# Kernel tuning notes

Hardware: AMD Instinct MI355X
Metric: run time of the kernel (lower is better)

## Reference

```python
import jax, jax.numpy as jnp
import numpy as np

NEG_SLOPE = 0.2


def _gat(x, src, dst, W, a_src, a_dst, b, N):
    # PyG GATConv (eval mode, concat=True). W: [Fin, H*C], a_*: [H, C], b: [H*C]
    H, C = a_src.shape
    h = (x @ W).reshape(N, H, C)                       # [N,H,C]
    al_s = jnp.einsum('nhc,hc->nh', h, a_src)          # source attention logits
    al_d = jnp.einsum('nhc,hc->nh', h, a_dst)          # target attention logits
    e = jax.nn.leaky_relu(al_s[src] + al_d[dst], NEG_SLOPE)  # [E,H]
    m = jax.ops.segment_max(e, dst, num_segments=N)
    m = jnp.where(jnp.isneginf(m), 0.0, m)
    p = jnp.exp(e - m[dst])
    s = jax.ops.segment_sum(p, dst, num_segments=N)
    alpha = p / (s[dst] + 1e-16)                       # segment softmax over incoming edges
    out = jax.ops.segment_sum(h[src] * alpha[:, :, None], dst, num_segments=N)
    return out.reshape(N, H * C) + b


def _lin(key, fin, fout):
    k1, k2 = jax.random.split(key)
    w = jax.random.normal(k1, (fin, fout), jnp.float32) / np.sqrt(fin)
    b = jax.random.normal(k2, (fout,), jnp.float32) * 0.01
    return w, b


def _gat_params(key, fin, H, C):
    k1, k2, k3, k4 = jax.random.split(key, 4)
    W = jax.random.normal(k1, (fin, H * C), jnp.float32) / np.sqrt(fin)
    a_s = jax.random.normal(k2, (H, C), jnp.float32) / np.sqrt(C)
    a_d = jax.random.normal(k3, (H, C), jnp.float32) / np.sqrt(C)
    b = jax.random.normal(k4, (H * C,), jnp.float32) * 0.01
    return W, a_s, a_d, b


def setup_inputs() -> dict:
    key = jax.random.key(0)
    N, E, F, HID, H = 20000, 320000, 128, 128, 2
    W_ = HID * H  # 256
    ks = jax.random.split(key, 12)
    x = jax.random.normal(ks[0], (N, F), jnp.float32)
    edge_index = jax.random.randint(ks[1], (2, E), 0, N, jnp.int64)
    edge_attr = jax.random.normal(ks[2], (E, 4), jnp.float32)
    ec_w1, ec_b1 = _lin(ks[3], 2 * F, HID)
    ec_w2, ec_b2 = _lin(ks[4], HID, HID)
    g1 = _gat_params(ks[5], HID, H, HID)
    g2 = _gat_params(ks[6], W_, H, HID)
    reg_w, reg_b = _lin(ks[7], W_, W_)
    g3 = _gat_params(ks[8], W_, H, HID)
    g4 = _gat_params(ks[9], W_, H, HID)
    fin_w, fin_b = _lin(ks[10], W_, 1)
    d = {"x": x, "edge_index": edge_index, "edge_attr": edge_attr,
         "ec_w1": ec_w1, "ec_b1": ec_b1, "ec_w2": ec_w2, "ec_b2": ec_b2,
         "reg_w": reg_w, "reg_b": reg_b, "fin_w": fin_w, "fin_b": fin_b}
    for name, p in (("g1", g1), ("g2", g2), ("g3", g3), ("g4", g4)):
        d[name + "_w"], d[name + "_as"], d[name + "_ad"], d[name + "_b"] = p
    return d


def reference(x, edge_index, edge_attr,
              ec_w1, ec_b1, ec_w2, ec_b2,
              g1_w, g1_as, g1_ad, g1_b,
              g2_w, g2_as, g2_ad, g2_b,
              reg_w, reg_b,
              g3_w, g3_as, g3_ad, g3_b,
              g4_w, g4_as, g4_ad, g4_b,
              fin_w, fin_b):
    N = x.shape[0]
    src, dst = edge_index[0], edge_index[1]
    # EdgeConv: msg = MLP([x_i, x_j - x_i]), max-aggregation at target i (no self loops)
    xi = x[dst]
    msg = jnp.concatenate([xi, x[src] - xi], axis=-1)          # [E, 2F]
    h = jnp.maximum(msg @ ec_w1 + ec_b1, 0.0) @ ec_w2 + ec_b2   # [E, HID]
    agg = jax.ops.segment_max(h, dst, num_segments=N)
    x = jnp.where(jnp.isneginf(agg), 0.0, agg)
    # GATConv adds self loops by default
    loop = jnp.arange(N, dtype=src.dtype)
    s2 = jnp.concatenate([src, loop])
    d2 = jnp.concatenate([dst, loop])
    # edge_attr is ignored by GATConv (edge_dim=None)
    x = jax.nn.relu(_gat(x, s2, d2, g1_w, g1_as, g1_ad, g1_b, N))
    r = x
    x = jax.nn.relu(_gat(x, s2, d2, g2_w, g2_as, g2_ad, g2_b, N)) + r
    x = x @ reg_w + reg_b
    r = x
    x = jax.nn.relu(_gat(x, s2, d2, g3_w, g3_as, g3_ad, g3_b, N)) + r
    x = jax.nn.relu(_gat(x, s2, d2, g4_w, g4_as, g4_ad, g4_b, N))
    return x @ fin_w + fin_b
```

## Files before the change

kernel.cpp:

```cpp
#include <hip/hip_runtime.h>
#include <math.h>


#define NEG_SLOPE 0.2f

typedef short short8 __attribute__((ext_vector_type(8)));
typedef float float4v __attribute__((ext_vector_type(4)));
typedef unsigned short ushort4v __attribute__((ext_vector_type(4)));

#define AS1 __attribute__((address_space(1)))
#define AS3 __attribute__((address_space(3)))

__device__ __forceinline__ void cp16(const void* g, void* l) {
  __builtin_amdgcn_global_load_lds((const AS1 unsigned int*)g, (AS3 unsigned int*)l, 16, 0, 0);
}

__device__ __forceinline__ float leaky(float x) { return x > 0.f ? x : NEG_SLOPE * x; }

__device__ __forceinline__ void atomicMaxF(float* addr, float v) {
  if (v >= 0.f) atomicMax((int*)addr, __float_as_int(v));
  else          atomicMin((unsigned int*)addr, __float_as_uint(v));
}

__device__ __forceinline__ unsigned short bf16_rn(float f) {
  unsigned u = __float_as_uint(f);
  unsigned r = (u + 0x7FFFu + ((u >> 16) & 1u)) >> 16;
  return (unsigned short)r;
}
__device__ __forceinline__ float bf16_to_f(unsigned short h) {
  return __uint_as_float(((unsigned)h) << 16);
}
__device__ __forceinline__ float4 ld_bf4(const unsigned short* p) {
  ushort4v u = *(const ushort4v*)p;
  float4 f;
  f.x = bf16_to_f(u[0]); f.y = bf16_to_f(u[1]);
  f.z = bf16_to_f(u[2]); f.w = bf16_to_f(u[3]);
  return f;
}

__global__ __launch_bounds__(256) void k_fill_f32(float* p, float v, int n) {
  int i = blockIdx.x * 256 + threadIdx.x;
  if (i < n) p[i] = v;
}

__global__ __launch_bounds__(256) void k_split_act(const float* __restrict__ src,
                                                   unsigned short* __restrict__ h,
                                                   unsigned short* __restrict__ l,
                                                   int n, int fixinf) {
  int i4 = (blockIdx.x * 256 + threadIdx.x) * 4;
  if (i4 >= n) return;
  float4 v = *(const float4*)&src[i4];
  if (fixinf) {
    if (v.x == -INFINITY) v.x = 0.f;
    if (v.y == -INFINITY) v.y = 0.f;
    if (v.z == -INFINITY) v.z = 0.f;
    if (v.w == -INFINITY) v.w = 0.f;
  }
  unsigned short hx = bf16_rn(v.x), hy = bf16_rn(v.y), hz = bf16_rn(v.z), hw = bf16_rn(v.w);
  ushort4v h4 = {hx, hy, hz, hw};
  ushort4v l4 = {bf16_rn(v.x - bf16_to_f(hx)), bf16_rn(v.y - bf16_to_f(hy)),
                 bf16_rn(v.z - bf16_to_f(hz)), bf16_rn(v.w - bf16_to_f(hw))};
  *(ushort4v*)&h[i4] = h4;
  *(ushort4v*)&l[i4] = l4;
}

__global__ __launch_bounds__(256) void k_hist(const int* __restrict__ ei, int* __restrict__ deg,
                                              int E) {
  int e = blockIdx.x * 256 + threadIdx.x;
  if (e < E) atomicAdd(&deg[ei[E + e]], 1);
}

__global__ __launch_bounds__(1024) void k_scan(const int* __restrict__ deg, int* __restrict__ rs,
                                               int n) {
  __shared__ int wsum[16];
  __shared__ int carry;
  int tid = threadIdx.x, lane = tid & 63, wv = tid >> 6;
  if (tid == 0) carry = 0;
  __syncthreads();
  for (int base = 0; base < n; base += 1024) {
    int i = base + tid;
    int v = (i < n) ? deg[i] : 0;
    int s = v;
    #pragma unroll
    for (int o = 1; o < 64; o <<= 1) {
      int t = __shfl(s, lane - o);
      if (lane >= o) s += t;
    }
    if (lane == 63) wsum[wv] = s;
    __syncthreads();
    if (wv == 0) {
      int x = (lane < 16) ? wsum[lane] : 0;
      #pragma unroll
      for (int o = 1; o < 16; o <<= 1) {
        int t = __shfl(x, lane - o);
        if (lane >= o) x += t;
      }
      if (lane < 16) wsum[lane] = x;
    }
    __syncthreads();
    int woff = carry + (wv ? wsum[wv - 1] : 0);
    if (i < n) rs[i] = woff + s - v;
    __syncthreads();
    if (tid == 0) carry += wsum[15];
    __syncthreads();
  }
  if (tid == 0) rs[n] = carry;
}

__global__ __launch_bounds__(256) void k_scatter(const int* __restrict__ ei,
                                                 const int* __restrict__ rs,
                                                 int* __restrict__ cnt,
                                                 int* __restrict__ csr_src,
                                                 int* __restrict__ csr_dst, int E) {
  int e = blockIdx.x * 256 + threadIdx.x;
  if (e < E) {
    int d = ei[E + e];
    int p = atomicAdd(&cnt[d], 1);
    int slot = rs[d] + p;
    csr_src[slot] = ei[e];
    csr_dst[slot] = d;
  }
}

struct SplitJob {
  const float* W;
  const float* aux;
  unsigned short* Th;
  unsigned short* Tl;
  float* bias_out;
  int K, N, kshift, type;
};
struct SplitJobs { SplitJob j[7]; };

__global__ __launch_bounds__(256) void k_prep_all(SplitJobs jobs) {
  SplitJob jb = jobs.j[blockIdx.y];
  int idx = blockIdx.x * 256 + threadIdx.x;
  if (idx >= jb.K * jb.N) return;
  float v;
  if (jb.type == 0) {
    int n = idx >> jb.kshift;
    int k = idx & (jb.K - 1);
    v = jb.W[k * jb.N + n];
  } else {
    int n = idx >> 7;
    int k = idx & 127;
    if (n < 128) v = jb.W[k * 128 + n] - jb.W[(k + 128) * 128 + n];
    else         v = jb.W[(k + 128) * 128 + (n - 128)];
    if (idx < 256) jb.bias_out[idx] = (idx < 128) ? jb.aux[idx] : 0.f;
  }
  unsigned short h = bf16_rn(v);
  jb.Th[idx] = h;
  jb.Tl[idx] = bf16_rn(v - bf16_to_f(h));
}

__global__ __launch_bounds__(256) void k_gemm_mfma(const unsigned short* __restrict__ Ah,
                                                   const unsigned short* __restrict__ Al,
                                                   const unsigned short* __restrict__ BTh,
                                                   const unsigned short* __restrict__ BTl,
                                                   const float* __restrict__ bias,
                                                   float* __restrict__ C, int M, int K,
                                                   unsigned short* __restrict__ Ch,
                                                   unsigned short* __restrict__ Cl,
                                                   unsigned short* __restrict__ Cbf,
                                                   const float* __restrict__ a_s,
                                                   const float* __restrict__ a_d,
                                                   float* __restrict__ al_out) {
  __shared__ __align__(16) char sm[24576];
  __shared__ float alS[64][2];
  char* AhS = sm;
  char* AlS = sm + 4096;
  char* BhS = sm + 8192;
  char* BlS = sm + 16384;

  const int tid = threadIdx.x;
  const int bm = blockIdx.x * 64;
  const int bn = blockIdx.y * 128;
  const int w = tid >> 6, lane = tid & 63, quad = lane >> 4, lr = lane & 15;
  const int kq8 = quad * 8;

  float4v zero4 = {0.f, 0.f, 0.f, 0.f};
  float4v acc[4][2];
  #pragma unroll
  for (int mt = 0; mt < 4; ++mt)
    #pragma unroll
    for (int nt = 0; nt < 2; ++nt) acc[mt][nt] = zero4;

  int ar = bm + w * 16 + lr; if (ar >= M) ar = M - 1;
  const size_t aoff  = (size_t)ar * K + kq8;
  const size_t boff0 = (size_t)(bn + (2 * w) * 16 + lr) * K + kq8;
  const size_t boff1 = (size_t)(bn + (2 * w + 1) * 16 + lr) * K + kq8;
  char* lA   = AhS + w * 1024;
  char* lAl  = AlS + w * 1024;
  char* lB0  = BhS + (2 * w) * 1024;
  char* lB1  = BhS + (2 * w + 1) * 1024;
  char* lBl0 = BlS + (2 * w) * 1024;
  char* lBl1 = BlS + (2 * w + 1) * 1024;

  for (int k0 = 0; k0 < K; k0 += 32) {
    __syncthreads();
    cp16(Ah + aoff + k0, lA);
    cp16(Al + aoff + k0, lAl);
    cp16(BTh + boff0 + k0, lB0);
    cp16(BTh + boff1 + k0, lB1);
    cp16(BTl + boff0 + k0, lBl0);
    cp16(BTl + boff1 + k0, lBl1);
    __syncthreads();
    short8 ah[4], alo[4], bh[2], blo[2];
    #pragma unroll
    for (int mt = 0; mt < 4; ++mt) {
      ah[mt]  = *(const short8*)(AhS + mt * 1024 + lane * 16);
      alo[mt] = *(const short8*)(AlS + mt * 1024 + lane * 16);
    }
    #pragma unroll
    for (int nt = 0; nt < 2; ++nt) {
      bh[nt]  = *(const short8*)(BhS + (2 * w + nt) * 1024 + lane * 16);
      blo[nt] = *(const short8*)(BlS + (2 * w + nt) * 1024 + lane * 16);
    }
    #pragma unroll
    for (int mt = 0; mt < 4; ++mt)
      #pragma unroll
      for (int nt = 0; nt < 2; ++nt) {
        acc[mt][nt] = __builtin_amdgcn_mfma_f32_16x16x32_bf16(ah[mt], bh[nt], acc[mt][nt], 0, 0, 0);
        acc[mt][nt] = __builtin_amdgcn_mfma_f32_16x16x32_bf16(alo[mt], bh[nt], acc[mt][nt], 0, 0, 0);
        acc[mt][nt] = __builtin_amdgcn_mfma_f32_16x16x32_bf16(ah[mt], blo[nt], acc[mt][nt], 0, 0, 0);
      }
  }
  #pragma unroll
  for (int nt = 0; nt < 2; ++nt) {
    int n = bn + w * 32 + nt * 16 + lr;
    float bv = bias ? bias[n] : 0.f;
    #pragma unroll
    for (int mt = 0; mt < 4; ++mt) {
      #pragma unroll
      for (int r = 0; r < 4; ++r) {
        int m = bm + mt * 16 + quad * 4 + r;
        if (m < M) {
          float v = acc[mt][nt][r] + bv;
          size_t idx = (size_t)m * 256 + n;
          if (C) C[idx] = v;
          if (Cbf) Cbf[idx] = bf16_rn(v);
          if (Ch) {
            unsigned short h = bf16_rn(v);
            Ch[idx] = h;
            Cl[idx] = bf16_rn(v - bf16_to_f(h));
          }
        }
      }
    }
  }
  if (a_s) {
    if (tid < 128) ((float*)alS)[tid] = 0.f;
    __syncthreads();
    float asv[2], adv[2];
    #pragma unroll
    for (int nt = 0; nt < 2; ++nt) {
      int n = bn + w * 32 + nt * 16 + lr;
      asv[nt] = a_s[n];
      adv[nt] = a_d[n];
    }
    #pragma unroll
    for (int mt = 0; mt < 4; ++mt) {
      #pragma unroll
      for (int r = 0; r < 4; ++r) {
        float ps = acc[mt][0][r] * asv[0] + acc[mt][1][r] * asv[1];
        float pd = acc[mt][0][r] * adv[0] + acc[mt][1][r] * adv[1];
        #pragma unroll
        for (int o = 8; o; o >>= 1) {
          ps += __shfl_xor(ps, o);
          pd += __shfl_xor(pd, o);
        }
        if (lr == 0) {
          int row = mt * 16 + quad * 4 + r;
          atomicAdd(&alS[row][0], ps);
          atomicAdd(&alS[row][1], pd);
        }
      }
    }
    __syncthreads();
    int head = bn >> 7;
    if (tid < 64) {
      int m = bm + tid;
      if (m < M) {
        al_out[m * 4 + head]     = alS[tid][0];
        al_out[m * 4 + 2 + head] = alS[tid][1];
      }
    }
  }
}

__global__ __launch_bounds__(256, 4) void k_edgeconv2(const float* __restrict__ uv,
                                                      const int* __restrict__ csr_src,
                                                      const int* __restrict__ csr_dst,
                                                      const unsigned short* __restrict__ w2Th,
                                                      const unsigned short* __restrict__ w2Tl,
                                                      const float* __restrict__ b2,
                                                      float* __restrict__ x0, int E) {
  __shared__ __align__(16) char smem[34816];
  unsigned short (*Ph)[136] = (unsigned short(*)[136])smem;
  unsigned short (*Pl)[136] = (unsigned short(*)[136])(smem + 17408);
  float (*H2)[132] = (float(*)[132])smem;
  __shared__ int sSrc[64], sDst[64];

  const int tid = threadIdx.x;
  const int e0 = blockIdx.x * 64;
  const int w = tid >> 6, lane = tid & 63, quad = lane >> 4, lr = lane & 15;
  if (tid < 64) {
    int e = e0 + tid;
    sSrc[tid] = (e < E) ? csr_src[e] : -1;
    sDst[tid] = (e < E) ? csr_dst[e] : -1;
  }
  __syncthreads();
  #pragma unroll
  for (int c = tid; c < 1024; c += 256) {
    int r = c >> 4;
    int kq = (c & 15) * 8;
    float pv[8];
    int sn = sSrc[r], dn = sDst[r];
    if (sn >= 0) {
      float4 u0 = *(const float4*)&uv[(size_t)dn * 256 + kq];
      float4 u1 = *(const float4*)&uv[(size_t)dn * 256 + kq + 4];
      float4 v0 = *(const float4*)&uv[(size_t)sn * 256 + 128 + kq];
      float4 v1 = *(const float4*)&uv[(size_t)sn * 256 + 128 + kq + 4];
      pv[0] = fmaxf(u0.x + v0.x, 0.f); pv[1] = fmaxf(u0.y + v0.y, 0.f);
      pv[2] = fmaxf(u0.z + v0.z, 0.f); pv[3] = fmaxf(u0.w + v0.w, 0.f);
      pv[4] = fmaxf(u1.x + v1.x, 0.f); pv[5] = fmaxf(u1.y + v1.y, 0.f);
      pv[6] = fmaxf(u1.z + v1.z, 0.f); pv[7] = fmaxf(u1.w + v1.w, 0.f);
    } else {
      #pragma unroll
      for (int i = 0; i < 8; ++i) pv[i] = 0.f;
    }
    short8 h8, l8;
    #pragma unroll
    for (int i = 0; i < 8; ++i) {
      unsigned short h = bf16_rn(pv[i]);
      h8[i] = (short)h;
      l8[i] = (short)bf16_rn(pv[i] - bf16_to_f(h));
    }
    *(short8*)&Ph[r][kq] = h8;
    *(short8*)&Pl[r][kq] = l8;
  }
  __syncthreads();
  float4v zero4 = {0.f, 0.f, 0.f, 0.f};
  float4v acc[4][2];
  #pragma unroll
  for (int mt = 0; mt < 4; ++mt)
    #pragma unroll
    for (int nt = 0; nt < 2; ++nt) acc[mt][nt] = zero4;

  #pragma unroll
  for (int k0 = 0; k0 < 128; k0 += 32) {
    short8 ah[4], alo[4], bh[2], blo[2];
    #pragma unroll
    for (int nt = 0; nt < 2; ++nt) {
      int n = w * 32 + nt * 16 + lr;
      bh[nt]  = *(const short8*)&w2Th[(size_t)n * 128 + k0 + quad * 8];
      blo[nt] = *(const short8*)&w2Tl[(size_t)n * 128 + k0 + quad * 8];
    }
    #pragma unroll
    for (int mt = 0; mt < 4; ++mt) {
      ah[mt]  = *(short8*)&Ph[mt * 16 + lr][k0 + quad * 8];
      alo[mt] = *(short8*)&Pl[mt * 16 + lr][k0 + quad * 8];
    }
    #pragma unroll
    for (int mt = 0; mt < 4; ++mt)
      #pragma unroll
      for (int nt = 0; nt < 2; ++nt) {
        acc[mt][nt] = __builtin_amdgcn_mfma_f32_16x16x32_bf16(ah[mt], bh[nt], acc[mt][nt], 0, 0, 0);
        acc[mt][nt] = __builtin_amdgcn_mfma_f32_16x16x32_bf16(alo[mt], bh[nt], acc[mt][nt], 0, 0, 0);
        acc[mt][nt] = __builtin_amdgcn_mfma_f32_16x16x32_bf16(ah[mt], blo[nt], acc[mt][nt], 0, 0, 0);
      }
  }
  __syncthreads();
  #pragma unroll
  for (int nt = 0; nt < 2; ++nt) {
    int n = w * 32 + nt * 16 + lr;
    float bv = b2[n];
    #pragma unroll
    for (int mt = 0; mt < 4; ++mt) {
      #pragma unroll
      for (int r = 0; r < 4; ++r) {
        int row = mt * 16 + quad * 4 + r;
        H2[row][n] = acc[mt][nt][r] + bv;
      }
    }
  }
  __syncthreads();
  {
    int half = tid >> 7;
    int col = tid & 127;
    int r0 = half * 32;
    int prev = sDst[r0];
    float rmax = H2[r0][col];
    for (int r = r0 + 1; r < r0 + 32; ++r) {
      int d = sDst[r];
      float v = H2[r][col];
      if (d == prev) {
        rmax = fmaxf(rmax, v);
      } else {
        if (prev >= 0) atomicMaxF(&x0[(size_t)prev * 128 + col], rmax);
        prev = d;
        rmax = v;
      }
    }
    if (prev >= 0) atomicMaxF(&x0[(size_t)prev * 128 + col], rmax);
  }
}

__global__ __launch_bounds__(256) void k_gat_agg(const unsigned short* __restrict__ Hfb,
                                                 const float* __restrict__ al,
                                                 const int* __restrict__ rs,
                                                 const int* __restrict__ csr_src,
                                                 const float* __restrict__ bias,
                                                 const float* __restrict__ res,
                                                 float* __restrict__ out,
                                                 unsigned short* __restrict__ outh,
                                                 unsigned short* __restrict__ outl,
                                                 const float* __restrict__ finw,
                                                 const float* __restrict__ finb, int N) {
  int wave = threadIdx.x >> 6, lane = threadIdx.x & 63;
  int i = blockIdx.x * 4 + wave;
  if (i >= N) return;
  int beg = rs[i], end = rs[i + 1];
  int deg = end - beg;
  float4 me = *(const float4*)&al[i * 4];
  float ad0 = me.z, ad1 = me.w;
  float sl0 = leaky(me.x + ad0);
  float sl1 = leaky(me.y + ad1);
  const int c = lane << 2;
  const int hsel = lane >> 5;
  float a0, a1, a2, a3;

  if (deg <= 64) {
    int s = 0;
    float l0 = -INFINITY, l1 = -INFINITY;
    bool act = lane < deg;
    if (act) {
      s = csr_src[beg + lane];
      float4 a4 = *(const float4*)&al[s * 4];
      l0 = leaky(a4.x + ad0);
      l1 = leaky(a4.y + ad1);
    }
    float m0 = fmaxf(sl0, l0), m1 = fmaxf(sl1, l1);
    #pragma unroll
    for (int o = 32; o; o >>= 1) {
      m0 = fmaxf(m0, __shfl_xor(m0, o));
      m1 = fmaxf(m1, __shfl_xor(m1, o));
    }
    float w0 = act ? __expf(l0 - m0) : 0.f;
    float w1 = act ? __expf(l1 - m1) : 0.f;
    float s0 = w0, s1 = w1;
    #pragma unroll
    for (int o = 32; o; o >>= 1) {
      s0 += __shfl_xor(s0, o);
      s1 += __shfl_xor(s1, o);
    }
    s0 += __expf(sl0 - m0);
    s1 += __expf(sl1 - m1);
    float inv0 = 1.f / (s0 + 1e-16f), inv1 = 1.f / (s1 + 1e-16f);
    float wp0 = w0 * inv0, wp1 = w1 * inv1;
    float wself = hsel ? __expf(sl1 - m1) * inv1 : __expf(sl0 - m0) * inv0;
    float4 hv = ld_bf4(&Hfb[(size_t)i * 256 + c]);
    a0 = wself * hv.x; a1 = wself * hv.y; a2 = wself * hv.z; a3 = wself * hv.w;
    float b0 = 0.f, b1 = 0.f, b2 = 0.f, b3 = 0.f;
    float c0 = 0.f, c1 = 0.f, c2 = 0.f, c3 = 0.f;
    float d0 = 0.f, d1 = 0.f, d2 = 0.f, d3 = 0.f;
    int j = 0;
    for (; j + 8 <= deg; j += 8) {
      int   sjj[8];
      float wjj[8];
      #pragma unroll
      for (int q = 0; q < 8; ++q) {
        sjj[q] = __shfl(s, j + q);
        float wA = __shfl(wp0, j + q);
        float wB = __shfl(wp1, j + q);
        wjj[q] = hsel ? wB : wA;
      }
      float4 h0 = ld_bf4(&Hfb[(size_t)sjj[0] * 256 + c]);
      float4 h1 = ld_bf4(&Hfb[(size_t)sjj[1] * 256 + c]);
      float4 h2 = ld_bf4(&Hfb[(size_t)sjj[2] * 256 + c]);
      float4 h3 = ld_bf4(&Hfb[(size_t)sjj[3] * 256 + c]);
      float4 h4 = ld_bf4(&Hfb[(size_t)sjj[4] * 256 + c]);
      float4 h5 = ld_bf4(&Hfb[(size_t)sjj[5] * 256 + c]);
      float4 h6 = ld_bf4(&Hfb[(size_t)sjj[6] * 256 + c]);
      float4 h7 = ld_bf4(&Hfb[(size_t)sjj[7] * 256 + c]);
      a0 += wjj[0] * h0.x; a1 += wjj[0] * h0.y; a2 += wjj[0] * h0.z; a3 += wjj[0] * h0.w;
      b0 += wjj[1] * h1.x; b1 += wjj[1] * h1.y; b2 += wjj[1] * h1.z; b3 += wjj[1] * h1.w;
      c0 += wjj[2] * h2.x; c1 += wjj[2] * h2.y; c2 += wjj[2] * h2.z; c3 += wjj[2] * h2.w;
      d0 += wjj[3] * h3.x; d1 += wjj[3] * h3.y; d2 += wjj[3] * h3.z; d3 += wjj[3] * h3.w;
      a0 += wjj[4] * h4.x; a1 += wjj[4] * h4.y; a2 += wjj[4] * h4.z; a3 += wjj[4] * h4.w;
      b0 += wjj[5] * h5.x; b1 += wjj[5] * h5.y; b2 += wjj[5] * h5.z; b3 += wjj[5] * h5.w;
      c0 += wjj[6] * h6.x; c1 += wjj[6] * h6.y; c2 += wjj[6] * h6.z; c3 += wjj[6] * h6.w;
      d0 += wjj[7] * h7.x; d1 += wjj[7] * h7.y; d2 += wjj[7] * h7.z; d3 += wjj[7] * h7.w;
    }
    for (; j < deg; ++j) {
      int sj = __shfl(s, j);
      float wA = __shfl(wp0, j);
      float wB = __shfl(wp1, j);
      float wj = hsel ? wB : wA;
      float4 h4 = ld_bf4(&Hfb[(size_t)sj * 256 + c]);
      a0 += wj * h4.x; a1 += wj * h4.y; a2 += wj * h4.z; a3 += wj * h4.w;
    }
    a0 += b0 + c0 + d0; a1 += b1 + c1 + d1;
    a2 += b2 + c2 + d2; a3 += b3 + c3 + d3;
  } else {
    float m0 = sl0, m1 = sl1;
    for (int e = beg + lane; e < end; e += 64) {
      int s = csr_src[e];
      m0 = fmaxf(m0, leaky(al[s * 4 + 0] + ad0));
      m1 = fmaxf(m1, leaky(al[s * 4 + 1] + ad1));
    }
    #pragma unroll
    for (int o = 32; o; o >>= 1) {
      m0 = fmaxf(m0, __shfl_xor(m0, o));
      m1 = fmaxf(m1, __shfl_xor(m1, o));
    }
    float s0 = 0.f, s1 = 0.f;
    for (int e = beg + lane; e < end; e += 64) {
      int s = csr_src[e];
      s0 += __expf(leaky(al[s * 4 + 0] + ad0) - m0);
      s1 += __expf(leaky(al[s * 4 + 1] + ad1) - m1);
    }
    #pragma unroll
    for (int o = 32; o; o >>= 1) {
      s0 += __shfl_xor(s0, o);
      s1 += __shfl_xor(s1, o);
    }
    s0 += __expf(sl0 - m0);
    s1 += __expf(sl1 - m1);
    float inv0 = 1.f / (s0 + 1e-16f), inv1 = 1.f / (s1 + 1e-16f);
    float mh = hsel ? m1 : m0;
    float invh = hsel ? inv1 : inv0;
    float adh = hsel ? ad1 : ad0;
    float wself = __expf((hsel ? sl1 : sl0) - mh) * invh;
    float4 hv = ld_bf4(&Hfb[(size_t)i * 256 + c]);
    a0 = wself * hv.x; a1 = wself * hv.y; a2 = wself * hv.z; a3 = wself * hv.w;
    for (int e = beg; e < end; ++e) {
      int s = csr_src[e];
      float wgt = __expf(leaky(al[s * 4 + hsel] + adh) - mh) * invh;
      float4 h4 = ld_bf4(&Hfb[(size_t)s * 256 + c]);
      a0 += wgt * h4.x; a1 += wgt * h4.y; a2 += wgt * h4.z; a3 += wgt * h4.w;
    }
  }
  float4 bv = *(const float4*)&bias[c];
  float4 o4;
  o4.x = fmaxf(a0 + bv.x, 0.f);
  o4.y = fmaxf(a1 + bv.y, 0.f);
  o4.z = fmaxf(a2 + bv.z, 0.f);
  o4.w = fmaxf(a3 + bv.w, 0.f);
  if (res) {
    float4 r4 = *(const float4*)&res[(size_t)i * 256 + c];
    o4.x += r4.x; o4.y += r4.y; o4.z += r4.z; o4.w += r4.w;
  }
  if (finw) {
    float4 wv = *(const float4*)&finw[c];
    float p = o4.x * wv.x + o4.y * wv.y + o4.z * wv.z + o4.w * wv.w;
    #pragma unroll
    for (int o = 32; o; o >>= 1) p += __shfl_xor(p, o);
    if (lane == 0) out[i] = p + finb[0];
    return;
  }
  size_t idx = (size_t)i * 256 + c;
  *(float4*)&out[idx] = o4;
  if (outh) {
    unsigned short hx = bf16_rn(o4.x), hy = bf16_rn(o4.y), hz = bf16_rn(o4.z), hw = bf16_rn(o4.w);
    ushort4v h4 = {hx, hy, hz, hw};
    ushort4v l4 = {bf16_rn(o4.x - bf16_to_f(hx)), bf16_rn(o4.y - bf16_to_f(hy)),
                   bf16_rn(o4.z - bf16_to_f(hz)), bf16_rn(o4.w - bf16_to_f(hw))};
    *(ushort4v*)&outh[idx] = h4;
    *(ushort4v*)&outl[idx] = l4;
  }
}

extern "C" void kernel_launch(void* const* d_in, const int* in_sizes, int n_in,
                              void* d_out, int out_size, void* d_ws, size_t ws_size,
                              hipStream_t stream) {
  const float* x      = (const float*)d_in[0];
  const int*   ei     = (const int*)d_in[1];
  const float* ec_w1  = (const float*)d_in[3];
  const float* ec_b1  = (const float*)d_in[4];
  const float* ec_w2  = (const float*)d_in[5];
  const float* ec_b2  = (const float*)d_in[6];
  const float* reg_w  = (const float*)d_in[7];
  const float* reg_b  = (const float*)d_in[8];
  const float* fin_w  = (const float*)d_in[9];
  const float* fin_b  = (const float*)d_in[10];
  const float* g1_w   = (const float*)d_in[11];
  const float* g1_as  = (const float*)d_in[12];
  const float* g1_ad  = (const float*)d_in[13];
  const float* g1_b   = (const float*)d_in[14];
  const float* g2_w   = (const float*)d_in[15];
  const float* g2_as  = (const float*)d_in[16];
  const float* g2_ad  = (const float*)d_in[17];
  const float* g2_b   = (const float*)d_in[18];
  const float* g3_w   = (const float*)d_in[19];
  const float* g3_as  = (const float*)d_in[20];
  const float* g3_ad  = (const float*)d_in[21];
  const float* g3_b   = (const float*)d_in[22];
  const float* g4_w   = (const float*)d_in[23];
  const float* g4_as  = (const float*)d_in[24];
  const float* g4_ad  = (const float*)d_in[25];
  const float* g4_b   = (const float*)d_in[26];

  const int N = in_sizes[0] / 128;
  const int E = in_sizes[1] / 2;

  char* base = (char*)d_ws;
  size_t off = 0;
  auto alloc = [&](size_t bytes) -> char* {
    char* p = base + off;
    off += (bytes + 255) & ~(size_t)255;
    return p;
  };
  const size_t szN4 = ((size_t)N * 4 + 255) & ~(size_t)255;
  int*   deg      = (int*)alloc((size_t)N * 4);
  int*   cnt      = (int*)alloc((size_t)N * 4);
  int*   rs       = (int*)alloc((size_t)(N + 1) * 4);
  int*   csr_src  = (int*)alloc((size_t)E * 4);
  int*   csr_dst  = (int*)alloc((size_t)E * 4);
  float* bias_cat = (float*)alloc(256 * 4);
  unsigned short* bcatTh = (unsigned short*)alloc(256 * 128 * 2);
  unsigned short* bcatTl = (unsigned short*)alloc(256 * 128 * 2);
  unsigned short* w2Th   = (unsigned short*)alloc(128 * 128 * 2);
  unsigned short* w2Tl   = (unsigned short*)alloc(128 * 128 * 2);
  unsigned short* g1Th   = (unsigned short*)alloc(256 * 128 * 2);
  unsigned short* g1Tl   = (unsigned short*)alloc(256 * 128 * 2);
  unsigned short* g2Th   = (unsigned short*)alloc(256 * 256 * 2);
  unsigned short* g2Tl   = (unsigned short*)alloc(256 * 256 * 2);
  unsigned short* g3Th   = (unsigned short*)alloc(256 * 256 * 2);
  unsigned short* g3Tl   = (unsigned short*)alloc(256 * 256 * 2);
  unsigned short* g4Th   = (unsigned short*)alloc(256 * 256 * 2);
  unsigned short* g4Tl   = (unsigned short*)alloc(256 * 256 * 2);
  unsigned short* regTh  = (unsigned short*)alloc(256 * 256 * 2);
  unsigned short* regTl  = (unsigned short*)alloc(256 * 256 * 2);
  float* uv  = (float*)alloc((size_t)N * 256 * 4);
  unsigned short* uvh = (unsigned short*)alloc((size_t)N * 256 * 2);
  float* x0 = (float*)alloc((size_t)N * 128 * 4);
  float* X1 = (float*)alloc((size_t)N * 256 * 4);
  float* X2 = (float*)alloc((size_t)N * 256 * 4);
  float* al = (float*)alloc((size_t)N * 4 * 4);
  unsigned short* s1h = (unsigned short*)alloc((size_t)N * 256 * 2);
  unsigned short* s1l = (unsigned short*)alloc((size_t)N * 256 * 2);
  unsigned short* s2h = (unsigned short*)alloc((size_t)N * 256 * 2);
  unsigned short* s2l = (unsigned short*)alloc((size_t)N * 256 * 2);
  (void)ws_size; (void)n_in; (void)out_size;

  const int nodeWaveBlocks = (N + 3) / 4;
  const dim3 gemmGrid((N + 63) / 64, 2);
  const int splitBlocks128 = (N * 128 / 4 + 255) / 256;

  SplitJobs jobs;
  jobs.j[0] = {ec_w2, nullptr, w2Th, w2Tl, nullptr, 128, 128, 7, 0};
  jobs.j[1] = {g1_w,  nullptr, g1Th, g1Tl, nullptr, 128, 256, 7, 0};
  jobs.j[2] = {g2_w,  nullptr, g2Th, g2Tl, nullptr, 256, 256, 8, 0};
  jobs.j[3] = {g3_w,  nullptr, g3Th, g3Tl, nullptr, 256, 256, 8, 0};
  jobs.j[4] = {g4_w,  nullptr, g4Th, g4Tl, nullptr, 256, 256, 8, 0};
  jobs.j[5] = {reg_w, nullptr, regTh, regTl, nullptr, 256, 256, 8, 0};
  jobs.j[6] = {ec_w1, ec_b1, bcatTh, bcatTl, bias_cat, 128, 256, 7, 1};
  k_prep_all<<<dim3(256, 7), 256, 0, stream>>>(jobs);

  hipMemsetAsync(deg, 0, 2 * szN4, stream);
  k_hist<<<(E + 255) / 256, 256, 0, stream>>>(ei, deg, E);
  k_scan<<<1, 1024, 0, stream>>>(deg, rs, N);
  k_scatter<<<(E + 255) / 256, 256, 0, stream>>>(ei, rs, cnt, csr_src, csr_dst, E);

  k_split_act<<<splitBlocks128, 256, 0, stream>>>(x, s1h, s1l, N * 128, 0);
  k_gemm_mfma<<<gemmGrid, 256, 0, stream>>>(s1h, s1l, bcatTh, bcatTl, bias_cat, uv, N, 128,
                                            nullptr, nullptr, nullptr,
                                            nullptr, nullptr, nullptr);
  k_fill_f32<<<(N * 128 + 255) / 256, 256, 0, stream>>>(x0, -INFINITY, N * 128);
  k_edgeconv2<<<(E + 63) / 64, 256, 0, stream>>>(uv, csr_src, csr_dst, w2Th, w2Tl, ec_b2, x0, E);
  k_split_act<<<splitBlocks128, 256, 0, stream>>>(x0, s1h, s1l, N * 128, 1);

  k_gemm_mfma<<<gemmGrid, 256, 0, stream>>>(s1h, s1l, g1Th, g1Tl, nullptr, nullptr, N, 128,
                                            nullptr, nullptr, uvh, g1_as, g1_ad, al);
  k_gat_agg<<<nodeWaveBlocks, 256, 0, stream>>>(uvh, al, rs, csr_src, g1_b, nullptr, X1,
                                                s1h, s1l, nullptr, nullptr, N);

  k_gemm_mfma<<<gemmGrid, 256, 0, stream>>>(s1h, s1l, g2Th, g2Tl, nullptr, nullptr, N, 256,
                                            nullptr, nullptr, uvh, g2_as, g2_ad, al);
  k_gat_agg<<<nodeWaveBlocks, 256, 0, stream>>>(uvh, al, rs, csr_src, g2_b, X1, X2,
                                                s2h, s2l, nullptr, nullptr, N);

  k_gemm_mfma<<<gemmGrid, 256, 0, stream>>>(s2h, s2l, regTh, regTl, reg_b, X1, N, 256,
                                            s1h, s1l, nullptr, nullptr, nullptr, nullptr);

  k_gemm_mfma<<<gemmGrid, 256, 0, stream>>>(s1h, s1l, g3Th, g3Tl, nullptr, nullptr, N, 256,
                                            nullptr, nullptr, uvh, g3_as, g3_ad, al);
  k_gat_agg<<<nodeWaveBlocks, 256, 0, stream>>>(uvh, al, rs, csr_src, g3_b, X1, X2,
                                                s2h, s2l, nullptr, nullptr, N);

  k_gemm_mfma<<<gemmGrid, 256, 0, stream>>>(s2h, s2l, g4Th, g4Tl, nullptr, nullptr, N, 256,
                                            nullptr, nullptr, uvh, g4_as, g4_ad, al);
  k_gat_agg<<<nodeWaveBlocks, 256, 0, stream>>>(uvh, al, rs, csr_src, g4_b, nullptr,
                                                (float*)d_out, nullptr, nullptr,
                                                fin_w, fin_b, N);
}
```

Before: 535.3 us.

## Halve GEMM N-tile to 64 and store per-quarter attention partials

The MFMA GEMM tile width drops from 128 to 64 columns and the grid grows from 2 to 4 column blocks. Each block now writes partial attention logits for its quarter into an 8-float per-node array. The GAT aggregation kernels load two float4s and add the two quarter partials per head. This doubles the number of blocks for better CU occupancy and lowers per-block LDS and registers, at the cost of reloading each A tile twice as often and reading twice as many attention bytes per edge in the gather-heavy aggregation.

```diff
diff --git a/kernel.cpp b/kernel.cpp
--- a/kernel.cpp
+++ b/kernel.cpp
@@ -165,69 +165,56 @@
                                                    const float* __restrict__ a_s,
                                                    const float* __restrict__ a_d,
                                                    float* __restrict__ al_out) {
-  __shared__ __align__(16) char sm[24576];
+  __shared__ __align__(16) char sm[16384];
   __shared__ float alS[64][2];
   char* AhS = sm;
   char* AlS = sm + 4096;
   char* BhS = sm + 8192;
-  char* BlS = sm + 16384;
+  char* BlS = sm + 12288;
 
   const int tid = threadIdx.x;
   const int bm = blockIdx.x * 64;
-  const int bn = blockIdx.y * 128;
+  const int bn = blockIdx.y * 64;
   const int w = tid >> 6, lane = tid & 63, quad = lane >> 4, lr = lane & 15;
   const int kq8 = quad * 8;
 
   float4v zero4 = {0.f, 0.f, 0.f, 0.f};
-  float4v acc[4][2];
+  float4v acc[4];
   #pragma unroll
-  for (int mt = 0; mt < 4; ++mt)
-    #pragma unroll
-    for (int nt = 0; nt < 2; ++nt) acc[mt][nt] = zero4;
+  for (int mt = 0; mt < 4; ++mt) acc[mt] = zero4;
 
   int ar = bm + w * 16 + lr; if (ar >= M) ar = M - 1;
-  const size_t aoff  = (size_t)ar * K + kq8;
-  const size_t boff0 = (size_t)(bn + (2 * w) * 16 + lr) * K + kq8;
-  const size_t boff1 = (size_t)(bn + (2 * w + 1) * 16 + lr) * K + kq8;
-  char* lA   = AhS + w * 1024;
-  char* lAl  = AlS + w * 1024;
-  char* lB0  = BhS + (2 * w) * 1024;
-  char* lB1  = BhS + (2 * w + 1) * 1024;
-  char* lBl0 = BlS + (2 * w) * 1024;
-  char* lBl1 = BlS + (2 * w + 1) * 1024;
+  const size_t aoff = (size_t)ar * K + kq8;
+  const size_t boff = (size_t)(bn + w * 16 + lr) * K + kq8;
+  char* lA  = AhS + w * 1024;
+  char* lAl = AlS + w * 1024;
+  char* lB  = BhS + w * 1024;
+  char* lBl = BlS + w * 1024;
 
   for (int k0 = 0; k0 < K; k0 += 32) {
     __syncthreads();
     cp16(Ah + aoff + k0, lA);
     cp16(Al + aoff + k0, lAl);
-    cp16(BTh + boff0 + k0, lB0);
-    cp16(BTh + boff1 + k0, lB1);
-    cp16(BTl + boff0 + k0, lBl0);
-    cp16(BTl + boff1 + k0, lBl1);
-    __syncthreads();
-    short8 ah[4], alo[4], bh[2], blo[2];
+    cp16(BTh + boff + k0, lB);
+    cp16(BTl + boff + k0, lBl);
+    __syncthreads();
+    short8 ah[4], alo[4], bh, blo;
     #pragma unroll
     for (int mt = 0; mt < 4; ++mt) {
       ah[mt]  = *(const short8*)(AhS + mt * 1024 + lane * 16);
       alo[mt] = *(const short8*)(AlS + mt * 1024 + lane * 16);
     }
-    #pragma unroll
-    for (int nt = 0; nt < 2; ++nt) {
-      bh[nt]  = *(const short8*)(BhS + (2 * w + nt) * 1024 + lane * 16);
-      blo[nt] = *(const short8*)(BlS + (2 * w + nt) * 1024 + lane * 16);
-    }
-    #pragma unroll
-    for (int mt = 0; mt < 4; ++mt)
-      #pragma unroll
-      for (int nt = 0; nt < 2; ++nt) {
-        acc[mt][nt] = __builtin_amdgcn_mfma_f32_16x16x32_bf16(ah[mt], bh[nt], acc[mt][nt], 0, 0, 0);
-        acc[mt][nt] = __builtin_amdgcn_mfma_f32_16x16x32_bf16(alo[mt], bh[nt], acc[mt][nt], 0, 0, 0);
-        acc[mt][nt] = __builtin_amdgcn_mfma_f32_16x16x32_bf16(ah[mt], blo[nt], acc[mt][nt], 0, 0, 0);
-      }
-  }
-  #pragma unroll
-  for (int nt = 0; nt < 2; ++nt) {
-    int n = bn + w * 32 + nt * 16 + lr;
+    bh  = *(const short8*)(BhS + w * 1024 + lane * 16);
+    blo = *(const short8*)(BlS + w * 1024 + lane * 16);
+    #pragma unroll
+    for (int mt = 0; mt < 4; ++mt) {
+      acc[mt] = __builtin_amdgcn_mfma_f32_16x16x32_bf16(ah[mt], bh, acc[mt], 0, 0, 0);
+      acc[mt] = __builtin_amdgcn_mfma_f32_16x16x32_bf16(alo[mt], bh, acc[mt], 0, 0, 0);
+      acc[mt] = __builtin_amdgcn_mfma_f32_16x16x32_bf16(ah[mt], blo, acc[mt], 0, 0, 0);
+    }
+  }
+  {
+    int n = bn + w * 16 + lr;
     float bv = bias ? bias[n] : 0.f;
     #pragma unroll
     for (int mt = 0; mt < 4; ++mt) {
@@ -235,7 +222,7 @@
       for (int r = 0; r < 4; ++r) {
         int m = bm + mt * 16 + quad * 4 + r;
         if (m < M) {
-          float v = acc[mt][nt][r] + bv;
+          float v = acc[mt][r] + bv;
           size_t idx = (size_t)m * 256 + n;
           if (C) C[idx] = v;
           if (Cbf) Cbf[idx] = bf16_rn(v);
@@ -251,19 +238,15 @@
   if (a_s) {
     if (tid < 128) ((float*)alS)[tid] = 0.f;
     __syncthreads();
-    float asv[2], adv[2];
-    #pragma unroll
-    for (int nt = 0; nt < 2; ++nt) {
-      int n = bn + w * 32 + nt * 16 + lr;
-      asv[nt] = a_s[n];
-      adv[nt] = a_d[n];
-    }
+    int n = bn + w * 16 + lr;
+    float asv = a_s[n];
+    float adv = a_d[n];
     #pragma unroll
     for (int mt = 0; mt < 4; ++mt) {
       #pragma unroll
       for (int r = 0; r < 4; ++r) {
-        float ps = acc[mt][0][r] * asv[0] + acc[mt][1][r] * asv[1];
-        float pd = acc[mt][0][r] * adv[0] + acc[mt][1][r] * adv[1];
+        float ps = acc[mt][r] * asv;
+        float pd = acc[mt][r] * adv;
         #pragma unroll
         for (int o = 8; o; o >>= 1) {
           ps += __shfl_xor(ps, o);
@@ -277,12 +260,12 @@
       }
     }
     __syncthreads();
-    int head = bn >> 7;
+    int q = blockIdx.y;
     if (tid < 64) {
       int m = bm + tid;
       if (m < M) {
-        al_out[m * 4 + head]     = alS[tid][0];
-        al_out[m * 4 + 2 + head] = alS[tid][1];
+        al_out[m * 8 + q * 2 + 0] = alS[tid][0];
+        al_out[m * 8 + q * 2 + 1] = alS[tid][1];
       }
     }
   }
@@ -422,10 +405,11 @@
   if (i >= N) return;
   int beg = rs[i], end = rs[i + 1];
   int deg = end - beg;
-  float4 me = *(const float4*)&al[i * 4];
-  float ad0 = me.z, ad1 = me.w;
-  float sl0 = leaky(me.x + ad0);
-  float sl1 = leaky(me.y + ad1);
+  float4 p0 = *(const float4*)&al[i * 8];
+  float4 p1 = *(const float4*)&al[i * 8 + 4];
+  float ad0 = p0.y + p0.w, ad1 = p1.y + p1.w;
+  float sl0 = leaky((p0.x + p0.z) + ad0);
+  float sl1 = leaky((p1.x + p1.z) + ad1);
   const int c = lane << 2;
   const int hsel = lane >> 5;
   float a0, a1, a2, a3;
@@ -436,9 +420,10 @@
     bool act = lane < deg;
     if (act) {
       s = csr_src[beg + lane];
-      float4 a4 = *(const float4*)&al[s * 4];
-      l0 = leaky(a4.x + ad0);
-      l1 = leaky(a4.y + ad1);
+      float4 q0 = *(const float4*)&al[s * 8];
+      float4 q1 = *(const float4*)&al[s * 8 + 4];
+      l0 = leaky((q0.x + q0.z) + ad0);
+      l1 = leaky((q1.x + q1.z) + ad1);
     }
     float m0 = fmaxf(sl0, l0), m1 = fmaxf(sl1, l1);
     #pragma unroll
@@ -506,8 +491,10 @@
     float m0 = sl0, m1 = sl1;
     for (int e = beg + lane; e < end; e += 64) {
       int s = csr_src[e];
-      m0 = fmaxf(m0, leaky(al[s * 4 + 0] + ad0));
-      m1 = fmaxf(m1, leaky(al[s * 4 + 1] + ad1));
+      float4 q0 = *(const float4*)&al[s * 8];
+      float4 q1 = *(const float4*)&al[s * 8 + 4];
+      m0 = fmaxf(m0, leaky((q0.x + q0.z) + ad0));
+      m1 = fmaxf(m1, leaky((q1.x + q1.z) + ad1));
     }
     #pragma unroll
     for (int o = 32; o; o >>= 1) {
@@ -517,8 +504,10 @@
     float s0 = 0.f, s1 = 0.f;
     for (int e = beg + lane; e < end; e += 64) {
       int s = csr_src[e];
-      s0 += __expf(leaky(al[s * 4 + 0] + ad0) - m0);
-      s1 += __expf(leaky(al[s * 4 + 1] + ad1) - m1);
+      float4 q0 = *(const float4*)&al[s * 8];
+      float4 q1 = *(const float4*)&al[s * 8 + 4];
+      s0 += __expf(leaky((q0.x + q0.z) + ad0) - m0);
+      s1 += __expf(leaky((q1.x + q1.z) + ad1) - m1);
     }
     #pragma unroll
     for (int o = 32; o; o >>= 1) {
@@ -536,7 +525,10 @@
     a0 = wself * hv.x; a1 = wself * hv.y; a2 = wself * hv.z; a3 = wself * hv.w;
     for (int e = beg; e < end; ++e) {
       int s = csr_src[e];
-      float wgt = __expf(leaky(al[s * 4 + hsel] + adh) - mh) * invh;
+      float4 q0 = *(const float4*)&al[s * 8];
+      float4 q1 = *(const float4*)&al[s * 8 + 4];
+      float lg = hsel ? leaky((q1.x + q1.z) + adh) : leaky((q0.x + q0.z) + adh);
+      float wgt = __expf(lg - mh) * invh;
       float4 h4 = ld_bf4(&Hfb[(size_t)s * 256 + c]);
       a0 += wgt * h4.x; a1 += wgt * h4.y; a2 += wgt * h4.z; a3 += wgt * h4.w;
     }
@@ -637,7 +629,7 @@
   float* x0 = (float*)alloc((size_t)N * 128 * 4);
   float* X1 = (float*)alloc((size_t)N * 256 * 4);
   float* X2 = (float*)alloc((size_t)N * 256 * 4);
-  float* al = (float*)alloc((size_t)N * 4 * 4);
+  float* al = (float*)alloc((size_t)N * 8 * 4);
   unsigned short* s1h = (unsigned short*)alloc((size_t)N * 256 * 2);
   unsigned short* s1l = (unsigned short*)alloc((size_t)N * 256 * 2);
   unsigned short* s2h = (unsigned short*)alloc((size_t)N * 256 * 2);
@@ -645,7 +637,7 @@
   (void)ws_size; (void)n_in; (void)out_size;
 
   const int nodeWaveBlocks = (N + 3) / 4;
-  const dim3 gemmGrid((N + 63) / 64, 2);
+  const dim3 gemmGrid((N + 63) / 64, 4);
   const int splitBlocks128 = (N * 128 / 4 + 255) / 256;
 
   SplitJobs jobs;
```

After: 551.2 us. 1.03x slower.

## Compose reg and GAT3 weights to remove dependent GEMM; truncate bf16 hi split

Applied to the files above, without the earlier changes.

Precomputes reg_w @ g3_w and the folded bias on device, so the GAT3 projection GEMM reads the GAT2 output directly instead of waiting for the reg GEMM's split activations. The reg GEMM now only writes the fp32 residual X1 and skips its hi/lo bf16 outputs. The GEMM's attention-logit epilogue now adds the bias, which the composed product needs. The hi/lo split also switches from round-to-nearest to truncation for the high half, saving a few ALU ops per element. The added work is a small serial-loop weight-compose kernel, and the changed association of products may shift numerics slightly.

```diff
diff --git a/kernel.cpp b/kernel.cpp
--- a/kernel.cpp
+++ b/kernel.cpp
@@ -29,6 +29,12 @@
 }
 __device__ __forceinline__ float bf16_to_f(unsigned short h) {
   return __uint_as_float(((unsigned)h) << 16);
+}
+__device__ __forceinline__ void split2(float v, unsigned short& h, unsigned short& l) {
+  unsigned u = __float_as_uint(v);
+  h = (unsigned short)(u >> 16);
+  float lo = v - __uint_as_float(u & 0xFFFF0000u);
+  l = bf16_rn(lo);
 }
 __device__ __forceinline__ float4 ld_bf4(const unsigned short* p) {
   ushort4v u = *(const ushort4v*)p;
@@ -56,10 +62,12 @@
     if (v.z == -INFINITY) v.z = 0.f;
     if (v.w == -INFINITY) v.w = 0.f;
   }
-  unsigned short hx = bf16_rn(v.x), hy = bf16_rn(v.y), hz = bf16_rn(v.z), hw = bf16_rn(v.w);
-  ushort4v h4 = {hx, hy, hz, hw};
-  ushort4v l4 = {bf16_rn(v.x - bf16_to_f(hx)), bf16_rn(v.y - bf16_to_f(hy)),
-                 bf16_rn(v.z - bf16_to_f(hz)), bf16_rn(v.w - bf16_to_f(hw))};
+  ushort4v h4, l4;
+  unsigned short th, tl;
+  split2(v.x, th, tl); h4[0] = th; l4[0] = tl;
+  split2(v.y, th, tl); h4[1] = th; l4[1] = tl;
+  split2(v.z, th, tl); h4[2] = th; l4[2] = tl;
+  split2(v.w, th, tl); h4[3] = th; l4[3] = tl;
   *(ushort4v*)&h[i4] = h4;
   *(ushort4v*)&l[i4] = l4;
 }
@@ -148,9 +156,32 @@
     else         v = jb.W[(k + 128) * 128 + (n - 128)];
     if (idx < 256) jb.bias_out[idx] = (idx < 128) ? jb.aux[idx] : 0.f;
   }
-  unsigned short h = bf16_rn(v);
+  unsigned short h, l;
+  split2(v, h, l);
   jb.Th[idx] = h;
-  jb.Tl[idx] = bf16_rn(v - bf16_to_f(h));
+  jb.Tl[idx] = l;
+}
+
+__global__ __launch_bounds__(256) void k_compose(const float* __restrict__ regw,
+                                                 const float* __restrict__ g3w,
+                                                 const float* __restrict__ regb,
+                                                 unsigned short* __restrict__ Th,
+                                                 unsigned short* __restrict__ Tl,
+                                                 float* __restrict__ biasC) {
+  int n = blockIdx.x;
+  int k = threadIdx.x;
+  float s = 0.f;
+  for (int j = 0; j < 256; ++j)
+    s += regw[k * 256 + j] * g3w[j * 256 + n];
+  unsigned short h, l;
+  split2(s, h, l);
+  Th[n * 256 + k] = h;
+  Tl[n * 256 + k] = l;
+  if (k == 0) {
+    float b = 0.f;
+    for (int j = 0; j < 256; ++j) b += regb[j] * g3w[j * 256 + n];
+    biasC[n] = b;
+  }
 }
 
 __global__ __launch_bounds__(256) void k_gemm_mfma(const unsigned short* __restrict__ Ah,
@@ -240,9 +271,10 @@
           if (C) C[idx] = v;
           if (Cbf) Cbf[idx] = bf16_rn(v);
           if (Ch) {
-            unsigned short h = bf16_rn(v);
+            unsigned short h, l;
+            split2(v, h, l);
             Ch[idx] = h;
-            Cl[idx] = bf16_rn(v - bf16_to_f(h));
+            Cl[idx] = l;
           }
         }
       }
@@ -251,19 +283,22 @@
   if (a_s) {
     if (tid < 128) ((float*)alS)[tid] = 0.f;
     __syncthreads();
-    float asv[2], adv[2];
+    float asv[2], adv[2], bvv[2];
     #pragma unroll
     for (int nt = 0; nt < 2; ++nt) {
       int n = bn + w * 32 + nt * 16 + lr;
       asv[nt] = a_s[n];
       adv[nt] = a_d[n];
+      bvv[nt] = bias ? bias[n] : 0.f;
     }
     #pragma unroll
     for (int mt = 0; mt < 4; ++mt) {
       #pragma unroll
       for (int r = 0; r < 4; ++r) {
-        float ps = acc[mt][0][r] * asv[0] + acc[mt][1][r] * asv[1];
-        float pd = acc[mt][0][r] * adv[0] + acc[mt][1][r] * adv[1];
+        float v0 = acc[mt][0][r] + bvv[0];
+        float v1 = acc[mt][1][r] + bvv[1];
+        float ps = v0 * asv[0] + v1 * asv[1];
+        float pd = v0 * adv[0] + v1 * adv[1];
         #pragma unroll
         for (int o = 8; o; o >>= 1) {
           ps += __shfl_xor(ps, o);
@@ -332,9 +367,10 @@
     short8 h8, l8;
     #pragma unroll
     for (int i = 0; i < 8; ++i) {
-      unsigned short h = bf16_rn(pv[i]);
+      unsigned short h, l;
+      split2(pv[i], h, l);
       h8[i] = (short)h;
-      l8[i] = (short)bf16_rn(pv[i] - bf16_to_f(h));
+      l8[i] = (short)l;
     }
     *(short8*)&Ph[r][kq] = h8;
     *(short8*)&Pl[r][kq] = l8;
@@ -562,10 +598,12 @@
   size_t idx = (size_t)i * 256 + c;
   *(float4*)&out[idx] = o4;
   if (outh) {
-    unsigned short hx = bf16_rn(o4.x), hy = bf16_rn(o4.y), hz = bf16_rn(o4.z), hw = bf16_rn(o4.w);
-    ushort4v h4 = {hx, hy, hz, hw};
-    ushort4v l4 = {bf16_rn(o4.x - bf16_to_f(hx)), bf16_rn(o4.y - bf16_to_f(hy)),
-                   bf16_rn(o4.z - bf16_to_f(hz)), bf16_rn(o4.w - bf16_to_f(hw))};
+    ushort4v h4, l4;
+    unsigned short th, tl;
+    split2(o4.x, th, tl); h4[0] = th; l4[0] = tl;
+    split2(o4.y, th, tl); h4[1] = th; l4[1] = tl;
+    split2(o4.z, th, tl); h4[2] = th; l4[2] = tl;
+    split2(o4.w, th, tl); h4[3] = th; l4[3] = tl;
     *(ushort4v*)&outh[idx] = h4;
     *(ushort4v*)&outl[idx] = l4;
   }
@@ -618,6 +656,7 @@
   int*   csr_src  = (int*)alloc((size_t)E * 4);
   int*   csr_dst  = (int*)alloc((size_t)E * 4);
   float* bias_cat = (float*)alloc(256 * 4);
+  float* biasC    = (float*)alloc(256 * 4);
   unsigned short* bcatTh = (unsigned short*)alloc(256 * 128 * 2);
   unsigned short* bcatTl = (unsigned short*)alloc(256 * 128 * 2);
   unsigned short* w2Th   = (unsigned short*)alloc(128 * 128 * 2);
@@ -632,6 +671,8 @@
   unsigned short* g4Tl   = (unsigned short*)alloc(256 * 256 * 2);
   unsigned short* regTh  = (unsigned short*)alloc(256 * 256 * 2);
   unsigned short* regTl  = (unsigned short*)alloc(256 * 256 * 2);
+  unsigned short* wcTh   = (unsigned short*)alloc(256 * 256 * 2);
+  unsigned short* wcTl   = (unsigned short*)alloc(256 * 256 * 2);
   float* uv  = (float*)alloc((size_t)N * 256 * 4);
   unsigned short* uvh = (unsigned short*)alloc((size_t)N * 256 * 2);
   float* x0 = (float*)alloc((size_t)N * 128 * 4);
@@ -657,6 +698,7 @@
   jobs.j[5] = {reg_w, nullptr, regTh, regTl, nullptr, 256, 256, 8, 0};
   jobs.j[6] = {ec_w1, ec_b1, bcatTh, bcatTl, bias_cat, 128, 256, 7, 1};
   k_prep_all<<<dim3(256, 7), 256, 0, stream>>>(jobs);
+  k_compose<<<256, 256, 0, stream>>>(reg_w, g3_w, reg_b, wcTh, wcTl, biasC);
 
   hipMemsetAsync(deg, 0, 2 * szN4, stream);
   k_hist<<<(E + 255) / 256, 256, 0, stream>>>(ei, deg, E);
@@ -682,9 +724,10 @@
                                                 s2h, s2l, nullptr, nullptr, N);
 
   k_gemm_mfma<<<gemmGrid, 256, 0, stream>>>(s2h, s2l, regTh, regTl, reg_b, X1, N, 256,
-                                            s1h, s1l, nullptr, nullptr, nullptr, nullptr);
-
-  k_gemm_mfma<<<gemmGrid, 256, 0, stream>>>(s1h, s1l, g3Th, g3Tl, nullptr, nullptr, N, 256,
+                                            nullptr, nullptr, nullptr,
+                                            nullptr, nullptr, nullptr);
+
+  k_gemm_mfma<<<gemmGrid, 256, 0, stream>>>(s2h, s2l, wcTh, wcTl, biasC, nullptr, N, 256,
                                             nullptr, nullptr, uvh, g3_as, g3_ad, al);
   k_gat_agg<<<nodeWaveBlocks, 256, 0, stream>>>(uvh, al, rs, csr_src, g3_b, X1, X2,
                                                 s2h, s2l, nullptr, nullptr, N);
```

Measured after the change: 555.3 us. 1.04x slower.
